# Kernel optimization log

Measured on AMD Instinct MI355X. Metric: run time of the kernel, lower is better.

The kernel has to match this reference:

```python
import jax, jax.numpy as jnp
import numpy as np

B, N, E_PER = 512, 256, 8192          # graphs, nodes per graph, edges per graph
FIN, H, K, FOUT = 128, 32, 16, 10     # in_channels, hidden, num clusters, out_channels
EPS = 1e-15


def setup_inputs() -> dict:
    key = jax.random.key(0)
    ks = jax.random.split(key, 12)
    x = jax.random.normal(ks[0], (B * N, FIN), jnp.float32)
    # intra-graph random edges, then offset into the global node index space
    src = jax.random.randint(ks[1], (B, E_PER), 0, N)
    dst = jax.random.randint(ks[2], (B, E_PER), 0, N)
    offs = (jnp.arange(B) * N)[:, None]
    edge_index = jnp.stack([(src + offs).reshape(-1), (dst + offs).reshape(-1)]).astype(jnp.int64)
    batch = jnp.repeat(jnp.arange(B), N).astype(jnp.int64)

    def lin(k, fin, fout):
        return (jax.random.normal(k, (fin, fout), jnp.float32) / np.sqrt(fin)).astype(jnp.float32)

    params = {
        'W_lin1': lin(ks[3], FIN, H), 'b_lin1': jnp.zeros((H,), jnp.float32),
        'W_rel1': lin(ks[4], H, H), 'b_rel1': jnp.zeros((H,), jnp.float32),
        'W_root1': lin(ks[5], H, H),
        'W_pool': lin(ks[6], H, K), 'b_pool': jnp.zeros((K,), jnp.float32),
        'W_rel2': lin(ks[7], H, H), 'b_rel2': jnp.zeros((H,), jnp.float32),
        'W_root2': lin(ks[8], H, H),
        'W_lin2': lin(ks[9], H, H), 'b_lin2': jnp.zeros((H,), jnp.float32),
        'W_lin3': lin(ks[10], H, FOUT), 'b_lin3': jnp.zeros((FOUT,), jnp.float32),
    }
    return {'x': x, 'edge_index': edge_index, 'batch': batch, **params}


def _densify(x, edge_index, batch):
    """to_dense_adj + to_dense_batch: [total,F] -> [B,N,F], [B,N,N], [B,N]."""
    n_total = x.shape[0]
    counts = jax.ops.segment_sum(jnp.ones((n_total,), jnp.int32), batch, num_segments=B)
    offsets = jnp.concatenate([jnp.zeros((1,), jnp.int32), jnp.cumsum(counts)[:-1]])
    pos = jnp.arange(n_total) - offsets[batch]            # position of node inside its graph
    eb = batch[edge_index[0]]                             # graph id of each edge
    adj = jnp.zeros((B, N, N), jnp.float32).at[eb, pos[edge_index[0]], pos[edge_index[1]]].add(1.0)
    xd = jnp.zeros((B, N, x.shape[1]), jnp.float32).at[batch, pos].set(x)
    mask = jnp.zeros((B, N), jnp.float32).at[batch, pos].set(1.0)
    return xd, adj, mask


def _dense_graph_conv(x, adj, W_rel, b_rel, W_root):
    # PyG DenseGraphConv(aggr='add'): lin_rel(adj @ x) + lin_root(x)
    return jnp.einsum('bnm,bmh,hk->bnk', adj, x, W_rel) + b_rel + x @ W_root


def _dense_mincut_pool(x, adj, s, mask):
    s = jax.nn.softmax(s, axis=-1)
    x = x * mask[..., None]
    s = s * mask[..., None]
    out = jnp.einsum('bnk,bnh->bkh', s, x)                        # s^T x
    out_adj = jnp.einsum('bnk,bnm,bmj->bkj', s, adj, s)           # s^T A s
    mincut_num = jnp.einsum('bkk->b', out_adj)
    d_flat = adj.sum(-1)                                          # degree
    mincut_den = jnp.einsum('bnk,bn,bnk->b', s, d_flat, s)        # trace(s^T D s)
    mincut_loss = jnp.mean(-(mincut_num / mincut_den))
    ss = jnp.einsum('bnk,bnj->bkj', s, s)
    ss_norm = jnp.linalg.norm(ss, axis=(-1, -2), keepdims=True)
    i_s = jnp.eye(K, dtype=jnp.float32)
    ortho_loss = jnp.mean(jnp.linalg.norm(ss / ss_norm - i_s / jnp.sqrt(jnp.float32(K)), axis=(-1, -2)))
    # zero diagonal, symmetric degree normalization
    diag_mask = 1.0 - i_s
    out_adj = out_adj * diag_mask
    d = jnp.sqrt(out_adj.sum(-1))[:, None, :] + EPS               # [B,1,K]
    out_adj = out_adj / d / jnp.swapaxes(d, 1, 2)
    return out, out_adj, mincut_loss, ortho_loss


def reference(x, edge_index, batch, W_lin1, b_lin1, W_rel1, b_rel1, W_root1,
              W_pool, b_pool, W_rel2, b_rel2, W_root2, W_lin2, b_lin2, W_lin3, b_lin3):
    xd, adj, mask = _densify(x, edge_index, batch)
    h = xd @ W_lin1 + b_lin1                                      # lin1
    h = _dense_graph_conv(h, adj, W_rel1, b_rel1, W_root1)        # conv1
    s2 = h @ W_pool + b_pool                                      # pool2
    h, adj_p, mincut_loss2, ortho_loss2 = _dense_mincut_pool(h, adj, s2, mask)
    h = _dense_graph_conv(h, adj_p, W_rel2, b_rel2, W_root2)      # conv2
    h = h.sum(axis=1)                                             # readout sum over clusters
    h = jax.nn.relu(h @ W_lin2 + b_lin2)
    h = h @ W_lin3 + b_lin3
    return jax.nn.log_softmax(h, axis=-1), mincut_loss2, ortho_loss2
```

## Files before the change

### kernel.cpp

```cpp
#include <hip/hip_runtime.h>

#define NB 512
#define NN 256
#define EPG 8192
#define FINC 128

typedef float f32x4 __attribute__((ext_vector_type(4)));
typedef short s16x8 __attribute__((ext_vector_type(8)));

__device__ __forceinline__ float bf2f(unsigned short u) {
  union { unsigned int i; float f; } x; x.i = ((unsigned int)u) << 16; return x.f;
}
__device__ __forceinline__ unsigned short f2bf(float f) {
  union { float f; unsigned int i; } x; x.f = f;
  unsigned int r = x.i + 0x7fffu + ((x.i >> 16) & 1u);
  return (unsigned short)(r >> 16);
}
__device__ __forceinline__ short ftrunc_bf(float f) {
  union { float f; unsigned int i; } x; x.f = f;
  return (short)(x.i >> 16);
}

struct Params {
  const void* x; const void* ei;
  const void *wl1, *bl1, *wr1, *br1, *wro1, *wp, *bp;
  const void *wr2, *br2, *wro2, *wl2, *bl2, *wl3, *bl3;
  float* out; float* ws;
};

__device__ __forceinline__ bool detect_bf16(const void* p) {
  const unsigned short* pw = (const unsigned short*)p;
  int sane = 0;
  for (int i = 0; i < 64; ++i) {
    unsigned e = (pw[i] >> 7) & 0xFFu;
    sane += (e > 96u && e < 132u) ? 1 : 0;
  }
  return sane >= 56;
}
__device__ __forceinline__ bool detect_i64(const void* p) {
  const int* pi = (const int*)p + EPG;
  int ok = 0;
  for (int i = 0; i < 32; ++i) ok += (pi[i] >= 256 && pi[i] < 512) ? 1 : 0;
  return ok < 24;
}
__device__ __forceinline__ float ldf(const void* p, int i, bool bf) {
  return bf ? bf2f(((const unsigned short*)p)[i]) : ((const float*)p)[i];
}

#define SMEM_TOTAL 162752

__global__ __launch_bounds__(1024, 4) void mincut_main(Params P) {
  extern __shared__ char smem[];
  const int t = threadIdx.x;
  const int b = blockIdx.x;

  const bool BF  = detect_bf16(P.wr1);
  const bool I64 = detect_i64(P.ei);

  float* h0buf  = (float*)(smem + 67584);
  unsigned short* taT = (unsigned short*)(smem + 67584);
  unsigned short* sTh = (unsigned short*)(smem + 76032);
  unsigned short* sTl = (unsigned short*)(smem + 84480);
  float* aggbuf = (float*)(smem + 104448);
  unsigned short* w1th = (unsigned short*)(smem + 104448);
  unsigned short* w1tl = (unsigned short*)(smem + 113152);
  unsigned short* h0T  = (unsigned short*)(smem + 141312);
  unsigned short* wrelTh  = (unsigned short*)(smem + 141312);
  unsigned short* wrelTl  = (unsigned short*)(smem + 143872);
  unsigned short* wrootTh = (unsigned short*)(smem + 146432);
  float* brel1f = (float*)(smem + 148992);
  unsigned short* h1Th = (unsigned short*)(smem + 141312);
  unsigned short* poolTh = (unsigned short*)(smem + 158208);
  unsigned short* poolTl = (unsigned short*)(smem + 159232);
  float* bpoolf = (float*)(smem + 160256);
  float* blin1f = (float*)(smem + 160320);
  float* scr    = (float*)(smem + 160448);
  float* degb   = (float*)(smem + 160704);
  float* ssqb   = (float*)(smem + 161728);
  float* pbuf   = (float*)(smem);
  float* oadjb  = (float*)(smem + 2048);
  float* ssb    = (float*)(smem + 3072);
  float* qbuf   = (float*)(smem + 4096);
  float* ddb    = (float*)(smem + 6144);
  float* h2b    = (float*)(smem + 6208);
  float* rb     = (float*)(smem + 8256);
  float* yb     = (float*)(smem + 8384);
  float* lgb    = (float*)(smem + 8512);
  float* rel2f  = (float*)(smem + 16384);
  float* root2f = (float*)(smem + 20608);
  float* lin2f  = (float*)(smem + 24704);
  float* lin3f  = (float*)(smem + 28928);
  float* pbufH  = (float*)(smem + 40960);
  float* pbufL  = (float*)(smem + 43008);
  float* oadjH  = (float*)(smem + 45056);
  float* oadjL  = (float*)(smem + 46080);
  float* ssA    = (float*)(smem + 47104);
  float* ssB    = (float*)(smem + 48128);
  float* ssC    = (float*)(smem + 49152);

  const int wv = t >> 6, lane = t & 63;
  const int lm = lane & 15, quad = lane >> 4;
  const int mbase = wv * 16;

  float wrel_v  = ldf(P.wr1, t, BF);
  float wroot_v = ldf(P.wro1, t, BF);
  float brel1_v = (t < 32) ? ldf(P.br1, t, BF) : 0.f;
  float rel2_v  = ldf(P.wr2, t, BF);
  float root2_v = ldf(P.wro2, t, BF);
  float lin2_v  = ldf(P.wl2, t, BF);
  float lin3_v  = (t < 320) ? ldf(P.wl3, t, BF) : 0.f;
  float brel2_v = (t < 32) ? ldf(P.br2, t, BF) : 0.f;
  float blin2_v = (t < 32) ? ldf(P.bl2, t, BF) : 0.f;
  float blin3_v = (t < 10) ? ldf(P.bl3, t, BF) : 0.f;
  int eu[8], ev[8];
  if (I64) {
    const uint4* s4 = (const uint4*)((const long long*)P.ei + (size_t)b * EPG) + t * 4;
    const uint4* d4 = (const uint4*)((const long long*)P.ei + (size_t)NB * EPG + (size_t)b * EPG) + t * 4;
    #pragma unroll
    for (int i = 0; i < 4; ++i) {
      uint4 a = s4[i], c = d4[i];
      eu[2 * i] = a.x & 255; eu[2 * i + 1] = a.z & 255;
      ev[2 * i] = c.x & 255; ev[2 * i + 1] = c.z & 255;
    }
  } else {
    const uint4* s4 = (const uint4*)((const int*)P.ei + (size_t)b * EPG) + t * 2;
    const uint4* d4 = (const uint4*)((const int*)P.ei + (size_t)NB * EPG + (size_t)b * EPG) + t * 2;
    #pragma unroll
    for (int i = 0; i < 2; ++i) {
      uint4 a = s4[i], c = d4[i];
      eu[4 * i] = a.x & 255; eu[4 * i + 1] = a.y & 255; eu[4 * i + 2] = a.z & 255; eu[4 * i + 3] = a.w & 255;
      ev[4 * i] = c.x & 255; ev[4 * i + 1] = c.y & 255; ev[4 * i + 2] = c.z & 255; ev[4 * i + 3] = c.w & 255;
    }
  }

  {
    uint4 z = {0u, 0u, 0u, 0u};
    for (int i = t; i < 4224; i += 1024) ((uint4*)smem)[i] = z;
  }
  for (int e = t; e < 4096; e += 1024) {
    int k = e >> 5, c = e & 31;
    float w = ldf(P.wl1, e, BF);
    unsigned short hi = f2bf(w);
    w1th[c * 136 + k] = hi;
    w1tl[c * 136 + k] = f2bf(w - bf2f(hi));
  }
  if (t < 512) {
    int m = t >> 4, c = t & 15;
    float w = ldf(P.wp, t, BF);
    unsigned short hi = f2bf(w);
    poolTh[c * 32 + m] = hi;
    poolTl[c * 32 + m] = f2bf(w - bf2f(hi));
  }
  if (t < 32) blin1f[t] = ldf(P.bl1, t, BF);
  if (t < 16) bpoolf[t] = ldf(P.bp, t, BF);
  __syncthreads();

  #pragma unroll
  for (int e = 0; e < 8; ++e) {
    unsigned idx = (unsigned)(eu[e] * 264 + ev[e]);
    atomicAdd((unsigned int*)(smem + (idx & ~3u)), 1u << ((idx & 3u) * 8u));
  }

  {
    f32x4 acc[2] = {{0.f,0.f,0.f,0.f},{0.f,0.f,0.f,0.f}};
    const size_t node = (size_t)(b * 256 + mbase + lm);
    #pragma unroll
    for (int ks = 0; ks < 4; ++ks) {
      const int k0 = ks * 32 + quad * 8;
      s16x8 a;
      if (BF) {
        a = *(const s16x8*)((const unsigned short*)P.x + node * 128 + k0);
      } else {
        const float* xp = (const float*)P.x + node * 128 + k0;
        f32x4 v0 = *(const f32x4*)xp;
        f32x4 v1 = *(const f32x4*)(xp + 4);
        #pragma unroll
        for (int j = 0; j < 4; ++j) { a[j] = (short)f2bf(v0[j]); a[4 + j] = (short)f2bf(v1[j]); }
      }
      #pragma unroll
      for (int ct = 0; ct < 2; ++ct) {
        const int c = ct * 16 + lm;
        s16x8 bh = *(const s16x8*)(w1th + c * 136 + k0);
        s16x8 bl = *(const s16x8*)(w1tl + c * 136 + k0);
        acc[ct] = __builtin_amdgcn_mfma_f32_16x16x32_bf16(a, bh, acc[ct], 0, 0, 0);
        acc[ct] = __builtin_amdgcn_mfma_f32_16x16x32_bf16(a, bl, acc[ct], 0, 0, 0);
      }
    }
    #pragma unroll
    for (int ct = 0; ct < 2; ++ct) {
      const int c = ct * 16 + lm;
      float bias = blin1f[c];
      #pragma unroll
      for (int r = 0; r < 4; ++r) {
        int row = mbase + quad * 4 + r;
        float val = acc[ct][r] + bias;
        h0buf[row * 36 + c] = val;
        h0T[c * 264 + row] = f2bf(val);
      }
    }
  }
  __syncthreads();

  s16x8 afr[8];
  {
    f32x4 acc[2] = {{0.f,0.f,0.f,0.f},{0.f,0.f,0.f,0.f}};
    float dsum = 0.f;
    const char* arow_ = smem + (mbase + lm) * 264;
    #pragma unroll
    for (int ks = 0; ks < 8; ++ks) {
      const int v0 = ks * 32 + quad * 8;
      uint2 d = *(const uint2*)(arow_ + v0);
      s16x8 a;
      #pragma unroll
      for (int j = 0; j < 4; ++j) {
        float f0 = (float)((d.x >> (8 * j)) & 255u);
        float f1 = (float)((d.y >> (8 * j)) & 255u);
        dsum += f0 + f1;
        a[j] = ftrunc_bf(f0);
        a[4 + j] = ftrunc_bf(f1);
      }
      afr[ks] = a;
      #pragma unroll
      for (int ct = 0; ct < 2; ++ct) {
        s16x8 bf = *(const s16x8*)(h0T + (ct * 16 + lm) * 264 + v0);
        acc[ct] = __builtin_amdgcn_mfma_f32_16x16x32_bf16(a, bf, acc[ct], 0, 0, 0);
      }
    }
    #pragma unroll
    for (int ct = 0; ct < 2; ++ct) {
      const int c = ct * 16 + lm;
      #pragma unroll
      for (int r = 0; r < 4; ++r) aggbuf[(mbase + quad * 4 + r) * 36 + c] = acc[ct][r];
    }
    dsum += __shfl_xor(dsum, 16, 64);
    dsum += __shfl_xor(dsum, 32, 64);
    if (lane < 16) degb[mbase + lm] = dsum;
  }
  __syncthreads();

  {
    int k = t >> 5, c = t & 31;
    unsigned short hi = f2bf(wrel_v);
    wrelTh[c * 40 + k] = hi;
    wrelTl[c * 40 + k] = f2bf(wrel_v - bf2f(hi));
    wrootTh[c * 40 + k] = f2bf(wroot_v);
  }
  if (t < 32) brel1f[t] = brel1_v;
  __syncthreads();

  f32x4 h1acc[2];
  float bias0, bias1;
  {
    s16x8 Ah, Al, Hh;
    const float* ar = aggbuf + (mbase + lm) * 36 + quad * 8;
    const float* hr = h0buf + (mbase + lm) * 36 + quad * 8;
    #pragma unroll
    for (int j = 0; j < 8; ++j) {
      float f = ar[j];
      unsigned short hi = f2bf(f);
      Ah[j] = (short)hi;
      Al[j] = (short)f2bf(f - bf2f(hi));
      Hh[j] = (short)f2bf(hr[j]);
    }
    bias0 = brel1f[lm]; bias1 = brel1f[16 + lm];
    #pragma unroll
    for (int ct = 0; ct < 2; ++ct) {
      const int c = ct * 16 + lm;
      s16x8 brh = *(const s16x8*)(wrelTh + c * 40 + quad * 8);
      s16x8 brl = *(const s16x8*)(wrelTl + c * 40 + quad * 8);
      s16x8 bwh = *(const s16x8*)(wrootTh + c * 40 + quad * 8);
      f32x4 acc = {0.f, 0.f, 0.f, 0.f};
      acc = __builtin_amdgcn_mfma_f32_16x16x32_bf16(Ah, brh, acc, 0, 0, 0);
      acc = __builtin_amdgcn_mfma_f32_16x16x32_bf16(Ah, brl, acc, 0, 0, 0);
      acc = __builtin_amdgcn_mfma_f32_16x16x32_bf16(Al, brh, acc, 0, 0, 0);
      acc = __builtin_amdgcn_mfma_f32_16x16x32_bf16(Hh, bwh, acc, 0, 0, 0);
      h1acc[ct] = acc;
    }
  }
  __syncthreads();
  {
    #pragma unroll
    for (int ct = 0; ct < 2; ++ct) {
      const int c = ct * 16 + lm;
      float bias = ct ? bias1 : bias0;
      #pragma unroll
      for (int r = 0; r < 4; ++r) {
        int row = mbase + quad * 4 + r;
        float val = h1acc[ct][r] + bias;
        aggbuf[row * 36 + c] = val;
        h1Th[c * 264 + row] = f2bf(val);
      }
    }
  }
  {
    s16x8 Ah, Al;
    const float* hr = aggbuf + (mbase + lm) * 36 + quad * 8;
    #pragma unroll
    for (int j = 0; j < 8; ++j) {
      float f = hr[j];
      unsigned short hi = f2bf(f);
      Ah[j] = (short)hi;
      Al[j] = (short)f2bf(f - bf2f(hi));
    }
    s16x8 Bh = *(const s16x8*)(poolTh + lm * 32 + quad * 8);
    s16x8 Bl = *(const s16x8*)(poolTl + lm * 32 + quad * 8);
    f32x4 lg = {0.f, 0.f, 0.f, 0.f};
    lg = __builtin_amdgcn_mfma_f32_16x16x32_bf16(Ah, Bh, lg, 0, 0, 0);
    lg = __builtin_amdgcn_mfma_f32_16x16x32_bf16(Al, Bh, lg, 0, 0, 0);
    lg = __builtin_amdgcn_mfma_f32_16x16x32_bf16(Ah, Bl, lg, 0, 0, 0);
    float bp = bpoolf[lm];
    #pragma unroll
    for (int r = 0; r < 4; ++r) lg[r] += bp;
    f32x4 mx = lg;
    #pragma unroll
    for (int m = 1; m <= 8; m <<= 1) {
      #pragma unroll
      for (int r = 0; r < 4; ++r) mx[r] = fmaxf(mx[r], __shfl_xor(mx[r], m, 64));
    }
    #pragma unroll
    for (int r = 0; r < 4; ++r) lg[r] = __expf(lg[r] - mx[r]);
    f32x4 sm = lg;
    #pragma unroll
    for (int m = 1; m <= 8; m <<= 1) {
      #pragma unroll
      for (int r = 0; r < 4; ++r) sm[r] += __shfl_xor(sm[r], m, 64);
    }
    f32x4 sq;
    #pragma unroll
    for (int r = 0; r < 4; ++r) {
      lg[r] = lg[r] / sm[r];
      sq[r] = lg[r] * lg[r];
    }
    #pragma unroll
    for (int m = 1; m <= 8; m <<= 1) {
      #pragma unroll
      for (int r = 0; r < 4; ++r) sq[r] += __shfl_xor(sq[r], m, 64);
    }
    #pragma unroll
    for (int r = 0; r < 4; ++r) {
      int node = mbase + quad * 4 + r;
      unsigned short hi = f2bf(lg[r]);
      sTh[lm * 264 + node] = hi;
      sTl[lm * 264 + node] = f2bf(lg[r] - bf2f(hi));
    }
    if (lm == 0) {
      #pragma unroll
      for (int r = 0; r < 4; ++r) ssqb[mbase + quad * 4 + r] = sq[r];
    }
  }
  __syncthreads();

  {
    f32x4 tacc = {0.f, 0.f, 0.f, 0.f};
    #pragma unroll
    for (int ks = 0; ks < 8; ++ks) {
      const int v0 = ks * 32 + quad * 8;
      s16x8 bh = *(const s16x8*)(sTh + lm * 264 + v0);
      s16x8 bl = *(const s16x8*)(sTl + lm * 264 + v0);
      tacc = __builtin_amdgcn_mfma_f32_16x16x32_bf16(afr[ks], bh, tacc, 0, 0, 0);
      tacc = __builtin_amdgcn_mfma_f32_16x16x32_bf16(afr[ks], bl, tacc, 0, 0, 0);
    }
    #pragma unroll
    for (int r = 0; r < 4; ++r) taT[lm * 264 + mbase + quad * 4 + r] = f2bf(tacc[r]);
  }
  __syncthreads();

  rel2f[t] = rel2_v;
  root2f[t] = root2_v;
  lin2f[t] = lin2_v;
  if (t < 320) lin3f[t] = lin3_v;

  if (wv < 9) {
    const unsigned short *Ap, *Bp; float* dst; int W, ct = 0;
    switch (wv) {
      case 0: Ap = sTh; Bp = h1Th; dst = pbufH; W = 32; ct = 0; break;
      case 1: Ap = sTh; Bp = h1Th; dst = pbufH; W = 32; ct = 1; break;
      case 2: Ap = sTl; Bp = h1Th; dst = pbufL; W = 32; ct = 0; break;
      case 3: Ap = sTl; Bp = h1Th; dst = pbufL; W = 32; ct = 1; break;
      case 4: Ap = sTh; Bp = taT;  dst = oadjH; W = 16; break;
      case 5: Ap = sTl; Bp = taT;  dst = oadjL; W = 16; break;
      case 6: Ap = sTh; Bp = sTh;  dst = ssA;   W = 16; break;
      case 7: Ap = sTh; Bp = sTl;  dst = ssB;   W = 16; break;
      default: Ap = sTl; Bp = sTh; dst = ssC;   W = 16; break;
    }
    const int cidx = ct * 16 + lm;
    const unsigned short* Bb = Bp + cidx * 264;
    f32x4 acc = {0.f, 0.f, 0.f, 0.f};
    #pragma unroll
    for (int ch = 0; ch < 8; ++ch) {
      s16x8 a = *(const s16x8*)(Ap + lm * 264 + ch * 32 + quad * 8);
      s16x8 bb = *(const s16x8*)(Bb + ch * 32 + quad * 8);
      acc = __builtin_amdgcn_mfma_f32_16x16x32_bf16(a, bb, acc, 0, 0, 0);
    }
    #pragma unroll
    for (int r = 0; r < 4; ++r) dst[(quad * 4 + r) * W + cidx] = acc[r];
  }
  __syncthreads();

  if (t < 512) {
    pbuf[t] = pbufH[t] + pbufL[t];
  } else if (t < 768) {
    int i = t - 512; oadjb[i] = oadjH[i] + oadjL[i];
  } else {
    int i = t - 768; ssb[i] = ssA[i] + ssB[i] + ssC[i];
  }
  __syncthreads();

  {
    float vden = (t < 256) ? degb[t] * ssqb[t] : 0.f;
    float vnum = (t < 16) ? oadjb[t * 17] : 0.f;
    float vfro = (t < 256) ? ssb[t] * ssb[t] : 0.f;
    float vtr  = (t < 16) ? ssb[t * 17] : 0.f;
    #pragma unroll
    for (int o = 32; o > 0; o >>= 1) {
      vden += __shfl_xor(vden, o, 64);
      vnum += __shfl_xor(vnum, o, 64);
      vfro += __shfl_xor(vfro, o, 64);
      vtr  += __shfl_xor(vtr, o, 64);
    }
    if (lane == 0) { scr[wv] = vden; scr[16 + wv] = vnum; scr[32 + wv] = vfro; scr[48 + wv] = vtr; }
  }
  __syncthreads();
  if (t == 0) {
    float den = 0.f, num = 0.f, fro = 0.f, tr = 0.f;
    #pragma unroll
    for (int i = 0; i < 16; ++i) { den += scr[i]; num += scr[16 + i]; fro += scr[32 + i]; tr += scr[48 + i]; }
    float ssn = sqrtf(fro);
    float orth2 = 2.f - tr / (2.f * ssn);
    atomicAdd(P.ws, -(num / den) * (1.f / NB));
    atomicAdd(P.ws + 1, sqrtf(fmaxf(orth2, 0.f)) * (1.f / NB));
  }
  if (t < 16) {
    float rs = 0.f;
    #pragma unroll
    for (int j = 0; j < 16; ++j) if (j != t) rs += oadjb[t * 16 + j];
    ddb[t] = sqrtf(rs) + 1e-15f;
  }
  __syncthreads();
  if (t < 256) {
    int k = t >> 4, j = t & 15;
    float apv = (k == j) ? 0.f : oadjb[t] / (ddb[k] * ddb[j]);
    oadjb[t] = apv;
  }
  __syncthreads();

  if (t < 512) {
    int k = t >> 5, c = t & 31;
    float q = 0.f;
    #pragma unroll
    for (int j = 0; j < 16; ++j) q += oadjb[k * 16 + j] * pbuf[j * 32 + c];
    qbuf[k * 32 + c] = q;
  }
  __syncthreads();
  if (t < 512) {
    int k = t >> 5, c = t & 31;
    float a1 = brel2_v;
    a1 = ((float*)nullptr == nullptr) ? a1 : a1;
    float acc = (t < 32) ? 0.f : 0.f;
    (void)acc;
    float s0 = 0.f;
    #pragma unroll
    for (int m = 0; m < 32; ++m)
      s0 += qbuf[k * 32 + m] * rel2f[m * 32 + c] + pbuf[k * 32 + m] * root2f[m * 32 + c];
    h2b[k * 32 + c] = s0;
  }
  __syncthreads();

  if (wv == 0) {
    if (lane < 32) {
      float r = 32.f * brel2_v;
      r = 0.f;
      #pragma unroll
      for (int k = 0; k < 16; ++k) r += h2b[k * 32 + lane];
      r += 16.f * brel2_v;
      rb[lane] = r;
    }
    if (lane < 32) {
      float y = blin2_v;
      #pragma unroll
      for (int m = 0; m < 32; ++m) y += rb[m] * lin2f[m * 32 + lane];
      yb[lane] = fmaxf(y, 0.f);
    }
    if (lane < 10) {
      float lg = blin3_v;
      #pragma unroll
      for (int m = 0; m < 32; ++m) lg += yb[m] * lin3f[m * 10 + lane];
      lgb[lane] = lg;
    }
    if (lane == 0) {
      float mx = lgb[0];
      #pragma unroll
      for (int i = 1; i < 10; ++i) mx = fmaxf(mx, lgb[i]);
      float sum = 0.f;
      #pragma unroll
      for (int i = 0; i < 10; ++i) sum += __expf(lgb[i] - mx);
      lgb[10] = mx + __logf(sum);
    }
    if (lane < 10) {
      float val = lgb[lane] - lgb[10];
      if (BF) ((unsigned short*)P.out)[b * 10 + lane] = f2bf(val);
      else    P.out[b * 10 + lane] = val;
    }
  }
}

__global__ void mincut_fin(Params P) {
  if (threadIdx.x == 0) {
    const bool BF = detect_bf16(P.wr1);
    if (BF) {
      ((unsigned short*)P.out)[5120] = f2bf(P.ws[0]);
      ((unsigned short*)P.out)[5121] = f2bf(P.ws[1]);
    } else {
      P.out[5120] = P.ws[0];
      P.out[5121] = P.ws[1];
    }
  }
}

extern "C" void kernel_launch(void* const* d_in, const int* in_sizes, int n_in,
                              void* d_out, int out_size, void* d_ws, size_t ws_size,
                              hipStream_t stream) {
  (void)in_sizes; (void)n_in; (void)out_size; (void)ws_size;
  Params P;
  P.x    = d_in[0];
  P.ei   = d_in[1];
  P.wl1  = d_in[3];
  P.bl1  = d_in[4];
  P.wr1  = d_in[5];
  P.br1  = d_in[6];
  P.wro1 = d_in[7];
  P.wp   = d_in[8];
  P.bp   = d_in[9];
  P.wr2  = d_in[10];
  P.br2  = d_in[11];
  P.wro2 = d_in[12];
  P.wl2  = d_in[13];
  P.bl2  = d_in[14];
  P.wl3  = d_in[15];
  P.bl3  = d_in[16];
  P.out  = (float*)d_out;
  P.ws   = (float*)d_ws;

  hipMemsetAsync(d_ws, 0, 2 * sizeof(float), stream);
  hipFuncSetAttribute(reinterpret_cast<const void*>(mincut_main),
                      hipFuncAttributeMaxDynamicSharedMemorySize, SMEM_TOTAL);
  hipLaunchKernelGGL(mincut_main, dim3(NB), dim3(1024), SMEM_TOTAL, stream, P);
  hipLaunchKernelGGL(mincut_fin, dim3(1), dim3(64), 0, stream, P);
}
```

Measured before the change: 182.6 us.

## Reassociate conv1 and pool via adjacency, pack adjacency as nibbles, halve LDS

Computes conv1 as A·(h0·Wrel) + h0·Wroot and the pool logits as A·(h0·Wrel·Wpool) + h0·Wroot·Wpool + bias, using precomputed weight products. The full-precision aggregation buffer and the separate conv1-to-pool stage go away. The adjacency is stored as 4-bit counts instead of 8-bit, and the ss terms are folded via symmetry. The lin1 split-bf16 low term is dropped. Shared memory shrinks from ~160KB to 80KB to allow two blocks per CU. Risks: counts above 15 overflow their nibble, and dropping the lin1 low term costs precision.

```diff
diff --git a/kernel.cpp b/kernel.cpp
--- a/kernel.cpp
+++ b/kernel.cpp
@@ -47,9 +47,9 @@
   return bf ? bf2f(((const unsigned short*)p)[i]) : ((const float*)p)[i];
 }
 
-#define SMEM_TOTAL 162752
-
-__global__ __launch_bounds__(1024, 4) void mincut_main(Params P) {
+#define SMEM_TOTAL 81920
+
+__global__ __launch_bounds__(1024, 8) void mincut_main(Params P) {
   extern __shared__ char smem[];
   const int t = threadIdx.x;
   const int b = blockIdx.x;
@@ -57,27 +57,7 @@
   const bool BF  = detect_bf16(P.wr1);
   const bool I64 = detect_i64(P.ei);
 
-  float* h0buf  = (float*)(smem + 67584);
-  unsigned short* taT = (unsigned short*)(smem + 67584);
-  unsigned short* sTh = (unsigned short*)(smem + 76032);
-  unsigned short* sTl = (unsigned short*)(smem + 84480);
-  float* aggbuf = (float*)(smem + 104448);
-  unsigned short* w1th = (unsigned short*)(smem + 104448);
-  unsigned short* w1tl = (unsigned short*)(smem + 113152);
-  unsigned short* h0T  = (unsigned short*)(smem + 141312);
-  unsigned short* wrelTh  = (unsigned short*)(smem + 141312);
-  unsigned short* wrelTl  = (unsigned short*)(smem + 143872);
-  unsigned short* wrootTh = (unsigned short*)(smem + 146432);
-  float* brel1f = (float*)(smem + 148992);
-  unsigned short* h1Th = (unsigned short*)(smem + 141312);
-  unsigned short* poolTh = (unsigned short*)(smem + 158208);
-  unsigned short* poolTl = (unsigned short*)(smem + 159232);
-  float* bpoolf = (float*)(smem + 160256);
-  float* blin1f = (float*)(smem + 160320);
-  float* scr    = (float*)(smem + 160448);
-  float* degb   = (float*)(smem + 160704);
-  float* ssqb   = (float*)(smem + 161728);
-  float* pbuf   = (float*)(smem);
+  float* pbuf   = (float*)(smem + 0);
   float* oadjb  = (float*)(smem + 2048);
   float* ssb    = (float*)(smem + 3072);
   float* qbuf   = (float*)(smem + 4096);
@@ -86,32 +66,45 @@
   float* rb     = (float*)(smem + 8256);
   float* yb     = (float*)(smem + 8384);
   float* lgb    = (float*)(smem + 8512);
-  float* rel2f  = (float*)(smem + 16384);
-  float* root2f = (float*)(smem + 20608);
-  float* lin2f  = (float*)(smem + 24704);
-  float* lin3f  = (float*)(smem + 28928);
-  float* pbufH  = (float*)(smem + 40960);
-  float* pbufL  = (float*)(smem + 43008);
-  float* oadjH  = (float*)(smem + 45056);
-  float* oadjL  = (float*)(smem + 46080);
-  float* ssA    = (float*)(smem + 47104);
-  float* ssB    = (float*)(smem + 48128);
-  float* ssC    = (float*)(smem + 49152);
+  float* scr    = (float*)(smem + 8704);
+  float* rel2f  = (float*)(smem + 9216);
+  float* root2f = (float*)(smem + 13312);
+  float* lin2f  = (float*)(smem + 17408);
+  float* lin3f  = (float*)(smem + 21504);
+  float* brel2f = (float*)(smem + 22784);
+  float* blin2f = (float*)(smem + 22912);
+  float* blin3f = (float*)(smem + 23040);
+  float* pbufH  = (float*)(smem + 24576);
+  float* pbufL  = (float*)(smem + 26624);
+  float* oadjH  = (float*)(smem + 28672);
+  float* oadjL  = (float*)(smem + 29696);
+  float* ssA    = (float*)(smem + 30720);
+  float* ssX    = (float*)(smem + 31744);
+  unsigned short* h0T  = (unsigned short*)(smem + 33792);
+  unsigned short* yTl  = (unsigned short*)(smem + 33792);
+  unsigned short* h1Th = (unsigned short*)(smem + 33792);
+  unsigned short* w1t  = (unsigned short*)(smem + 50688);
+  unsigned short* zT   = (unsigned short*)(smem + 50688);
+  unsigned short* sTh  = (unsigned short*)(smem + 50688);
+  unsigned short* sTl  = (unsigned short*)(smem + 59136);
+  unsigned short* wrelTh = (unsigned short*)(smem + 67584);
+  unsigned short* wrelTl = (unsigned short*)(smem + 70144);
+  unsigned short* wrootT = (unsigned short*)(smem + 72704);
+  float* blin1f = (float*)(smem + 75264);
+  unsigned short* yTh = (unsigned short*)(smem + 67584);
+  unsigned short* taT = (unsigned short*)(smem + 67584);
+  unsigned short* wpoolTh = (unsigned short*)(smem + 76032);
+  unsigned short* wpoolTl = (unsigned short*)(smem + 77184);
+  unsigned short* m1Th    = (unsigned short*)(smem + 78336);
+  unsigned short* m1Tl    = (unsigned short*)(smem + 79488);
+  unsigned short* m2Th    = (unsigned short*)(smem + 80640);
+  float*          bMf     = (float*)(smem + 81792);
+  unsigned short* brel1h  = (unsigned short*)(smem + 81856);
 
   const int wv = t >> 6, lane = t & 63;
   const int lm = lane & 15, quad = lane >> 4;
   const int mbase = wv * 16;
 
-  float wrel_v  = ldf(P.wr1, t, BF);
-  float wroot_v = ldf(P.wro1, t, BF);
-  float brel1_v = (t < 32) ? ldf(P.br1, t, BF) : 0.f;
-  float rel2_v  = ldf(P.wr2, t, BF);
-  float root2_v = ldf(P.wro2, t, BF);
-  float lin2_v  = ldf(P.wl2, t, BF);
-  float lin3_v  = (t < 320) ? ldf(P.wl3, t, BF) : 0.f;
-  float brel2_v = (t < 32) ? ldf(P.br2, t, BF) : 0.f;
-  float blin2_v = (t < 32) ? ldf(P.bl2, t, BF) : 0.f;
-  float blin3_v = (t < 10) ? ldf(P.bl3, t, BF) : 0.f;
   int eu[8], ev[8];
   if (I64) {
     const uint4* s4 = (const uint4*)((const long long*)P.ei + (size_t)b * EPG) + t * 4;
@@ -135,30 +128,34 @@
 
   {
     uint4 z = {0u, 0u, 0u, 0u};
-    for (int i = t; i < 4224; i += 1024) ((uint4*)smem)[i] = z;
+    for (int i = t; i < 2112; i += 1024) ((uint4*)smem)[i] = z;
   }
   for (int e = t; e < 4096; e += 1024) {
     int k = e >> 5, c = e & 31;
-    float w = ldf(P.wl1, e, BF);
-    unsigned short hi = f2bf(w);
-    w1th[c * 136 + k] = hi;
-    w1tl[c * 136 + k] = f2bf(w - bf2f(hi));
+    w1t[c * 136 + k] = f2bf(ldf(P.wl1, e, BF));
+  }
+  {
+    int k = t >> 5, c = t & 31;
+    float wr = ldf(P.wr1, t, BF);
+    unsigned short hi = f2bf(wr);
+    wrelTh[c * 40 + k] = hi;
+    wrelTl[c * 40 + k] = f2bf(wr - bf2f(hi));
+    wrootT[c * 40 + k] = f2bf(ldf(P.wro1, t, BF));
   }
   if (t < 512) {
     int m = t >> 4, c = t & 15;
     float w = ldf(P.wp, t, BF);
     unsigned short hi = f2bf(w);
-    poolTh[c * 32 + m] = hi;
-    poolTl[c * 32 + m] = f2bf(w - bf2f(hi));
-  }
-  if (t < 32) blin1f[t] = ldf(P.bl1, t, BF);
-  if (t < 16) bpoolf[t] = ldf(P.bp, t, BF);
+    wpoolTh[c * 36 + m] = hi;
+    wpoolTl[c * 36 + m] = f2bf(w - bf2f(hi));
+  }
+  if (t < 32) { blin1f[t] = ldf(P.bl1, t, BF); brel1h[t] = f2bf(ldf(P.br1, t, BF)); }
   __syncthreads();
 
   #pragma unroll
   for (int e = 0; e < 8; ++e) {
-    unsigned idx = (unsigned)(eu[e] * 264 + ev[e]);
-    atomicAdd((unsigned int*)(smem + (idx & ~3u)), 1u << ((idx & 3u) * 8u));
+    unsigned nib = (unsigned)(eu[e] * 264 + ev[e]);
+    atomicAdd((unsigned int*)(smem + ((nib >> 3) << 2)), 1u << ((nib & 7u) * 4u));
   }
 
   {
@@ -179,11 +176,8 @@
       }
       #pragma unroll
       for (int ct = 0; ct < 2; ++ct) {
-        const int c = ct * 16 + lm;
-        s16x8 bh = *(const s16x8*)(w1th + c * 136 + k0);
-        s16x8 bl = *(const s16x8*)(w1tl + c * 136 + k0);
+        s16x8 bh = *(const s16x8*)(w1t + (ct * 16 + lm) * 136 + k0);
         acc[ct] = __builtin_amdgcn_mfma_f32_16x16x32_bf16(a, bh, acc[ct], 0, 0, 0);
-        acc[ct] = __builtin_amdgcn_mfma_f32_16x16x32_bf16(a, bl, acc[ct], 0, 0, 0);
       }
     }
     #pragma unroll
@@ -191,162 +185,179 @@
       const int c = ct * 16 + lm;
       float bias = blin1f[c];
       #pragma unroll
-      for (int r = 0; r < 4; ++r) {
-        int row = mbase + quad * 4 + r;
-        float val = acc[ct][r] + bias;
-        h0buf[row * 36 + c] = val;
-        h0T[c * 264 + row] = f2bf(val);
-      }
-    }
-  }
-  __syncthreads();
-
-  s16x8 afr[8];
-  {
-    f32x4 acc[2] = {{0.f,0.f,0.f,0.f},{0.f,0.f,0.f,0.f}};
-    float dsum = 0.f;
-    const char* arow_ = smem + (mbase + lm) * 264;
-    #pragma unroll
-    for (int ks = 0; ks < 8; ++ks) {
-      const int v0 = ks * 32 + quad * 8;
-      uint2 d = *(const uint2*)(arow_ + v0);
-      s16x8 a;
-      #pragma unroll
-      for (int j = 0; j < 4; ++j) {
-        float f0 = (float)((d.x >> (8 * j)) & 255u);
-        float f1 = (float)((d.y >> (8 * j)) & 255u);
-        dsum += f0 + f1;
-        a[j] = ftrunc_bf(f0);
-        a[4 + j] = ftrunc_bf(f1);
-      }
-      afr[ks] = a;
-      #pragma unroll
-      for (int ct = 0; ct < 2; ++ct) {
-        s16x8 bf = *(const s16x8*)(h0T + (ct * 16 + lm) * 264 + v0);
-        acc[ct] = __builtin_amdgcn_mfma_f32_16x16x32_bf16(a, bf, acc[ct], 0, 0, 0);
-      }
-    }
-    #pragma unroll
-    for (int ct = 0; ct < 2; ++ct) {
-      const int c = ct * 16 + lm;
-      #pragma unroll
-      for (int r = 0; r < 4; ++r) aggbuf[(mbase + quad * 4 + r) * 36 + c] = acc[ct][r];
-    }
-    dsum += __shfl_xor(dsum, 16, 64);
-    dsum += __shfl_xor(dsum, 32, 64);
-    if (lane < 16) degb[mbase + lm] = dsum;
-  }
-  __syncthreads();
-
-  {
-    int k = t >> 5, c = t & 31;
-    unsigned short hi = f2bf(wrel_v);
-    wrelTh[c * 40 + k] = hi;
-    wrelTl[c * 40 + k] = f2bf(wrel_v - bf2f(hi));
-    wrootTh[c * 40 + k] = f2bf(wroot_v);
-  }
-  if (t < 32) brel1f[t] = brel1_v;
-  __syncthreads();
-
-  f32x4 h1acc[2];
-  float bias0, bias1;
-  {
-    s16x8 Ah, Al, Hh;
-    const float* ar = aggbuf + (mbase + lm) * 36 + quad * 8;
-    const float* hr = h0buf + (mbase + lm) * 36 + quad * 8;
+      for (int r = 0; r < 4; ++r)
+        h0T[c * 264 + mbase + quad * 4 + r] = f2bf(acc[ct][r] + bias);
+    }
+  }
+
+  if (wv == 2 || wv == 3) {
+    const int mb = (wv - 2) * 16;
+    s16x8 Ah, Al;
     #pragma unroll
     for (int j = 0; j < 8; ++j) {
-      float f = ar[j];
-      unsigned short hi = f2bf(f);
-      Ah[j] = (short)hi;
-      Al[j] = (short)f2bf(f - bf2f(hi));
-      Hh[j] = (short)f2bf(hr[j]);
-    }
-    bias0 = brel1f[lm]; bias1 = brel1f[16 + lm];
+      int k = quad * 8 + j;
+      Ah[j] = (short)wrelTh[k * 40 + mb + lm];
+      Al[j] = (short)wrelTl[k * 40 + mb + lm];
+    }
+    s16x8 Bh, Bl;
+    ((uint2*)&Bh)[0] = *(const uint2*)(wpoolTh + lm * 36 + quad * 8);
+    ((uint2*)&Bh)[1] = *(const uint2*)(wpoolTh + lm * 36 + quad * 8 + 4);
+    ((uint2*)&Bl)[0] = *(const uint2*)(wpoolTl + lm * 36 + quad * 8);
+    ((uint2*)&Bl)[1] = *(const uint2*)(wpoolTl + lm * 36 + quad * 8 + 4);
+    f32x4 acc = {0.f, 0.f, 0.f, 0.f};
+    acc = __builtin_amdgcn_mfma_f32_16x16x32_bf16(Ah, Bh, acc, 0, 0, 0);
+    acc = __builtin_amdgcn_mfma_f32_16x16x32_bf16(Al, Bh, acc, 0, 0, 0);
+    acc = __builtin_amdgcn_mfma_f32_16x16x32_bf16(Ah, Bl, acc, 0, 0, 0);
+    #pragma unroll
+    for (int r = 0; r < 4; ++r) {
+      int m = mb + quad * 4 + r;
+      unsigned short hi = f2bf(acc[r]);
+      m1Th[lm * 36 + m] = hi;
+      m1Tl[lm * 36 + m] = f2bf(acc[r] - bf2f(hi));
+    }
+  }
+  if (wv == 4 || wv == 5) {
+    const int mb = (wv - 4) * 16;
+    s16x8 Ah;
+    #pragma unroll
+    for (int j = 0; j < 8; ++j) Ah[j] = (short)wrootT[(quad * 8 + j) * 40 + mb + lm];
+    s16x8 Bh, Bl;
+    ((uint2*)&Bh)[0] = *(const uint2*)(wpoolTh + lm * 36 + quad * 8);
+    ((uint2*)&Bh)[1] = *(const uint2*)(wpoolTh + lm * 36 + quad * 8 + 4);
+    ((uint2*)&Bl)[0] = *(const uint2*)(wpoolTl + lm * 36 + quad * 8);
+    ((uint2*)&Bl)[1] = *(const uint2*)(wpoolTl + lm * 36 + quad * 8 + 4);
+    f32x4 acc = {0.f, 0.f, 0.f, 0.f};
+    acc = __builtin_amdgcn_mfma_f32_16x16x32_bf16(Ah, Bh, acc, 0, 0, 0);
+    acc = __builtin_amdgcn_mfma_f32_16x16x32_bf16(Ah, Bl, acc, 0, 0, 0);
+    #pragma unroll
+    for (int r = 0; r < 4; ++r) m2Th[lm * 36 + (mb + quad * 4 + r)] = f2bf(acc[r]);
+  }
+  if (wv == 6 && lane < 16) {
+    float acc = ldf(P.bp, lane, BF);
+    #pragma unroll 8
+    for (int m = 0; m < 32; ++m)
+      acc += bf2f(brel1h[m]) * (bf2f(wpoolTh[lane * 36 + m]) + bf2f(wpoolTl[lane * 36 + m]));
+    bMf[lane] = acc;
+  }
+  __syncthreads();
+
+  f32x4 racc[2] = {{0.f,0.f,0.f,0.f},{0.f,0.f,0.f,0.f}};
+  f32x4 yacc = {0.f,0.f,0.f,0.f}, macc = {0.f,0.f,0.f,0.f};
+  {
+    s16x8 Ah;
+    #pragma unroll
+    for (int j = 0; j < 8; ++j) Ah[j] = (short)h0T[(quad * 8 + j) * 264 + mbase + lm];
+    f32x4 zacc[2] = {{0.f,0.f,0.f,0.f},{0.f,0.f,0.f,0.f}};
     #pragma unroll
     for (int ct = 0; ct < 2; ++ct) {
       const int c = ct * 16 + lm;
       s16x8 brh = *(const s16x8*)(wrelTh + c * 40 + quad * 8);
       s16x8 brl = *(const s16x8*)(wrelTl + c * 40 + quad * 8);
-      s16x8 bwh = *(const s16x8*)(wrootTh + c * 40 + quad * 8);
-      f32x4 acc = {0.f, 0.f, 0.f, 0.f};
-      acc = __builtin_amdgcn_mfma_f32_16x16x32_bf16(Ah, brh, acc, 0, 0, 0);
-      acc = __builtin_amdgcn_mfma_f32_16x16x32_bf16(Ah, brl, acc, 0, 0, 0);
-      acc = __builtin_amdgcn_mfma_f32_16x16x32_bf16(Al, brh, acc, 0, 0, 0);
-      acc = __builtin_amdgcn_mfma_f32_16x16x32_bf16(Hh, bwh, acc, 0, 0, 0);
-      h1acc[ct] = acc;
-    }
-  }
-  __syncthreads();
-  {
+      s16x8 bro = *(const s16x8*)(wrootT + c * 40 + quad * 8);
+      zacc[ct] = __builtin_amdgcn_mfma_f32_16x16x32_bf16(Ah, brh, zacc[ct], 0, 0, 0);
+      zacc[ct] = __builtin_amdgcn_mfma_f32_16x16x32_bf16(Ah, brl, zacc[ct], 0, 0, 0);
+      racc[ct] = __builtin_amdgcn_mfma_f32_16x16x32_bf16(Ah, bro, racc[ct], 0, 0, 0);
+    }
+    s16x8 Bm1h, Bm1l, Bm2;
+    ((uint2*)&Bm1h)[0] = *(const uint2*)(m1Th + lm * 36 + quad * 8);
+    ((uint2*)&Bm1h)[1] = *(const uint2*)(m1Th + lm * 36 + quad * 8 + 4);
+    ((uint2*)&Bm1l)[0] = *(const uint2*)(m1Tl + lm * 36 + quad * 8);
+    ((uint2*)&Bm1l)[1] = *(const uint2*)(m1Tl + lm * 36 + quad * 8 + 4);
+    ((uint2*)&Bm2)[0]  = *(const uint2*)(m2Th + lm * 36 + quad * 8);
+    ((uint2*)&Bm2)[1]  = *(const uint2*)(m2Th + lm * 36 + quad * 8 + 4);
+    yacc = __builtin_amdgcn_mfma_f32_16x16x32_bf16(Ah, Bm1h, yacc, 0, 0, 0);
+    yacc = __builtin_amdgcn_mfma_f32_16x16x32_bf16(Ah, Bm1l, yacc, 0, 0, 0);
+    macc = __builtin_amdgcn_mfma_f32_16x16x32_bf16(Ah, Bm2, macc, 0, 0, 0);
+    #pragma unroll
+    for (int ct = 0; ct < 2; ++ct)
+      #pragma unroll
+      for (int r = 0; r < 4; ++r)
+        zT[(ct * 16 + lm) * 264 + mbase + quad * 4 + r] = f2bf(zacc[ct][r]);
+  }
+  __syncthreads();
+
+  #pragma unroll
+  for (int r = 0; r < 4; ++r) {
+    int node = mbase + quad * 4 + r;
+    unsigned short hi = f2bf(yacc[r]);
+    yTh[lm * 264 + node] = hi;
+    yTl[lm * 264 + node] = f2bf(yacc[r] - bf2f(hi));
+  }
+  __syncthreads();
+
+  unsigned adjw[8];
+  f32x4 h1v[2], sval, sq;
+  float degf;
+  {
+    f32x4 h1acc[2] = {{0.f,0.f,0.f,0.f},{0.f,0.f,0.f,0.f}};
+    f32x4 lacc = {0.f,0.f,0.f,0.f};
+    unsigned dsum = 0;
+    const char* arow = smem + (mbase + lm) * 132;
+    #pragma unroll
+    for (int ks = 0; ks < 8; ++ks) {
+      unsigned d = *(const unsigned int*)(arow + ks * 16 + quad * 4);
+      adjw[ks] = d;
+      unsigned v = (d & 0x0F0F0F0Fu) + ((d >> 4) & 0x0F0F0F0Fu);
+      dsum += (v * 0x01010101u) >> 24;
+      s16x8 af;
+      #pragma unroll
+      for (int j = 0; j < 8; ++j) af[j] = ftrunc_bf((float)((d >> (4 * j)) & 15u));
+      const int v0 = ks * 32 + quad * 8;
+      #pragma unroll
+      for (int ct = 0; ct < 2; ++ct) {
+        s16x8 bz = *(const s16x8*)(zT + (ct * 16 + lm) * 264 + v0);
+        h1acc[ct] = __builtin_amdgcn_mfma_f32_16x16x32_bf16(af, bz, h1acc[ct], 0, 0, 0);
+      }
+      s16x8 byh = *(const s16x8*)(yTh + lm * 264 + v0);
+      s16x8 byl = *(const s16x8*)(yTl + lm * 264 + v0);
+      lacc = __builtin_amdgcn_mfma_f32_16x16x32_bf16(af, byh, lacc, 0, 0, 0);
+      lacc = __builtin_amdgcn_mfma_f32_16x16x32_bf16(af, byl, lacc, 0, 0, 0);
+    }
+    dsum += __shfl_xor(dsum, 16, 64);
+    dsum += __shfl_xor(dsum, 32, 64);
+    degf = (float)dsum;
     #pragma unroll
     for (int ct = 0; ct < 2; ++ct) {
-      const int c = ct * 16 + lm;
-      float bias = ct ? bias1 : bias0;
-      #pragma unroll
-      for (int r = 0; r < 4; ++r) {
-        int row = mbase + quad * 4 + r;
-        float val = h1acc[ct][r] + bias;
-        aggbuf[row * 36 + c] = val;
-        h1Th[c * 264 + row] = f2bf(val);
-      }
-    }
-  }
-  {
-    s16x8 Ah, Al;
-    const float* hr = aggbuf + (mbase + lm) * 36 + quad * 8;
-    #pragma unroll
-    for (int j = 0; j < 8; ++j) {
-      float f = hr[j];
-      unsigned short hi = f2bf(f);
-      Ah[j] = (short)hi;
-      Al[j] = (short)f2bf(f - bf2f(hi));
-    }
-    s16x8 Bh = *(const s16x8*)(poolTh + lm * 32 + quad * 8);
-    s16x8 Bl = *(const s16x8*)(poolTl + lm * 32 + quad * 8);
-    f32x4 lg = {0.f, 0.f, 0.f, 0.f};
-    lg = __builtin_amdgcn_mfma_f32_16x16x32_bf16(Ah, Bh, lg, 0, 0, 0);
-    lg = __builtin_amdgcn_mfma_f32_16x16x32_bf16(Al, Bh, lg, 0, 0, 0);
-    lg = __builtin_amdgcn_mfma_f32_16x16x32_bf16(Ah, Bl, lg, 0, 0, 0);
-    float bp = bpoolf[lm];
-    #pragma unroll
-    for (int r = 0; r < 4; ++r) lg[r] += bp;
+      float bias = bf2f(brel1h[ct * 16 + lm]);
+      #pragma unroll
+      for (int r = 0; r < 4; ++r) h1v[ct][r] = h1acc[ct][r] + racc[ct][r] + bias;
+    }
+    f32x4 lg;
+    float bm = bMf[lm];
+    #pragma unroll
+    for (int r = 0; r < 4; ++r) lg[r] = lacc[r] + macc[r] + bm;
     f32x4 mx = lg;
     #pragma unroll
-    for (int m = 1; m <= 8; m <<= 1) {
+    for (int m = 1; m <= 8; m <<= 1)
       #pragma unroll
       for (int r = 0; r < 4; ++r) mx[r] = fmaxf(mx[r], __shfl_xor(mx[r], m, 64));
-    }
     #pragma unroll
     for (int r = 0; r < 4; ++r) lg[r] = __expf(lg[r] - mx[r]);
     f32x4 sm = lg;
     #pragma unroll
-    for (int m = 1; m <= 8; m <<= 1) {
+    for (int m = 1; m <= 8; m <<= 1)
       #pragma unroll
       for (int r = 0; r < 4; ++r) sm[r] += __shfl_xor(sm[r], m, 64);
-    }
-    f32x4 sq;
-    #pragma unroll
-    for (int r = 0; r < 4; ++r) {
-      lg[r] = lg[r] / sm[r];
-      sq[r] = lg[r] * lg[r];
-    }
-    #pragma unroll
-    for (int m = 1; m <= 8; m <<= 1) {
+    #pragma unroll
+    for (int r = 0; r < 4; ++r) { sval[r] = lg[r] / sm[r]; sq[r] = sval[r] * sval[r]; }
+    #pragma unroll
+    for (int m = 1; m <= 8; m <<= 1)
       #pragma unroll
       for (int r = 0; r < 4; ++r) sq[r] += __shfl_xor(sq[r], m, 64);
-    }
-    #pragma unroll
-    for (int r = 0; r < 4; ++r) {
-      int node = mbase + quad * 4 + r;
-      unsigned short hi = f2bf(lg[r]);
-      sTh[lm * 264 + node] = hi;
-      sTl[lm * 264 + node] = f2bf(lg[r] - bf2f(hi));
-    }
-    if (lm == 0) {
-      #pragma unroll
-      for (int r = 0; r < 4; ++r) ssqb[mbase + quad * 4 + r] = sq[r];
-    }
+  }
+  __syncthreads();
+
+  #pragma unroll
+  for (int ct = 0; ct < 2; ++ct)
+    #pragma unroll
+    for (int r = 0; r < 4; ++r)
+      h1Th[(ct * 16 + lm) * 264 + mbase + quad * 4 + r] = f2bf(h1v[ct][r]);
+  #pragma unroll
+  for (int r = 0; r < 4; ++r) {
+    int node = mbase + quad * 4 + r;
+    unsigned short hi = f2bf(sval[r]);
+    sTh[lm * 264 + node] = hi;
+    sTl[lm * 264 + node] = f2bf(sval[r] - bf2f(hi));
   }
   __syncthreads();
 
@@ -354,23 +365,30 @@
     f32x4 tacc = {0.f, 0.f, 0.f, 0.f};
     #pragma unroll
     for (int ks = 0; ks < 8; ++ks) {
+      unsigned d = adjw[ks];
+      s16x8 af;
+      #pragma unroll
+      for (int j = 0; j < 8; ++j) af[j] = ftrunc_bf((float)((d >> (4 * j)) & 15u));
       const int v0 = ks * 32 + quad * 8;
       s16x8 bh = *(const s16x8*)(sTh + lm * 264 + v0);
       s16x8 bl = *(const s16x8*)(sTl + lm * 264 + v0);
-      tacc = __builtin_amdgcn_mfma_f32_16x16x32_bf16(afr[ks], bh, tacc, 0, 0, 0);
-      tacc = __builtin_amdgcn_mfma_f32_16x16x32_bf16(afr[ks], bl, tacc, 0, 0, 0);
+      tacc = __builtin_amdgcn_mfma_f32_16x16x32_bf16(af, bh, tacc, 0, 0, 0);
+      tacc = __builtin_amdgcn_mfma_f32_16x16x32_bf16(af, bl, tacc, 0, 0, 0);
     }
     #pragma unroll
     for (int r = 0; r < 4; ++r) taT[lm * 264 + mbase + quad * 4 + r] = f2bf(tacc[r]);
   }
   __syncthreads();
 
-  rel2f[t] = rel2_v;
-  root2f[t] = root2_v;
-  lin2f[t] = lin2_v;
-  if (t < 320) lin3f[t] = lin3_v;
-
-  if (wv < 9) {
+  rel2f[t] = ldf(P.wr2, t, BF);
+  root2f[t] = ldf(P.wro2, t, BF);
+  lin2f[t] = ldf(P.wl2, t, BF);
+  if (t < 320) lin3f[t] = ldf(P.wl3, t, BF);
+  if (t < 32) brel2f[t] = ldf(P.br2, t, BF);
+  if (t < 32) blin2f[t] = ldf(P.bl2, t, BF);
+  if (t < 10) blin3f[t] = ldf(P.bl3, t, BF);
+
+  if (wv < 8) {
     const unsigned short *Ap, *Bp; float* dst; int W, ct = 0;
     switch (wv) {
       case 0: Ap = sTh; Bp = h1Th; dst = pbufH; W = 32; ct = 0; break;
@@ -380,8 +398,7 @@
       case 4: Ap = sTh; Bp = taT;  dst = oadjH; W = 16; break;
       case 5: Ap = sTl; Bp = taT;  dst = oadjL; W = 16; break;
       case 6: Ap = sTh; Bp = sTh;  dst = ssA;   W = 16; break;
-      case 7: Ap = sTh; Bp = sTl;  dst = ssB;   W = 16; break;
-      default: Ap = sTl; Bp = sTh; dst = ssC;   W = 16; break;
+      default: Ap = sTh; Bp = sTl; dst = ssX;   W = 16; break;
     }
     const int cidx = ct * 16 + lm;
     const unsigned short* Bb = Bp + cidx * 264;
@@ -402,12 +419,17 @@
   } else if (t < 768) {
     int i = t - 512; oadjb[i] = oadjH[i] + oadjL[i];
   } else {
-    int i = t - 768; ssb[i] = ssA[i] + ssB[i] + ssC[i];
-  }
-  __syncthreads();
-
-  {
-    float vden = (t < 256) ? degb[t] * ssqb[t] : 0.f;
+    int i = t - 768; int k3 = i >> 4, j3 = i & 15;
+    ssb[i] = ssA[i] + ssX[i] + ssX[j3 * 16 + k3];
+  }
+  __syncthreads();
+
+  {
+    int l = lane & 15, src = (l >> 2) << 4;
+    float q0 = __shfl(sq[0], src, 64), q1 = __shfl(sq[1], src, 64);
+    float q2 = __shfl(sq[2], src, 64), q3 = __shfl(sq[3], src, 64);
+    float ssel = (l & 2) ? ((l & 1) ? q3 : q2) : ((l & 1) ? q1 : q0);
+    float vden = (lane < 16) ? degf * ssel : 0.f;
     float vnum = (t < 16) ? oadjb[t * 17] : 0.f;
     float vfro = (t < 256) ? ssb[t] * ssb[t] : 0.f;
     float vtr  = (t < 16) ? ssb[t * 17] : 0.f;
@@ -421,6 +443,7 @@
     if (lane == 0) { scr[wv] = vden; scr[16 + wv] = vnum; scr[32 + wv] = vfro; scr[48 + wv] = vtr; }
   }
   __syncthreads();
+
   if (t == 0) {
     float den = 0.f, num = 0.f, fro = 0.f, tr = 0.f;
     #pragma unroll
@@ -454,10 +477,6 @@
   __syncthreads();
   if (t < 512) {
     int k = t >> 5, c = t & 31;
-    float a1 = brel2_v;
-    a1 = ((float*)nullptr == nullptr) ? a1 : a1;
-    float acc = (t < 32) ? 0.f : 0.f;
-    (void)acc;
     float s0 = 0.f;
     #pragma unroll
     for (int m = 0; m < 32; ++m)
@@ -468,21 +487,19 @@
 
   if (wv == 0) {
     if (lane < 32) {
-      float r = 32.f * brel2_v;
-      r = 0.f;
+      float r = 16.f * brel2f[lane];
       #pragma unroll
       for (int k = 0; k < 16; ++k) r += h2b[k * 32 + lane];
-      r += 16.f * brel2_v;
       rb[lane] = r;
     }
     if (lane < 32) {
-      float y = blin2_v;
+      float y = blin2f[lane];
       #pragma unroll
       for (int m = 0; m < 32; ++m) y += rb[m] * lin2f[m * 32 + lane];
       yb[lane] = fmaxf(y, 0.f);
     }
     if (lane < 10) {
-      float lg = blin3_v;
+      float lg = blin3f[lane];
       #pragma unroll
       for (int m = 0; m < 32; ++m) lg += yb[m] * lin3f[m * 10 + lane];
       lgb[lane] = lg;
```

After: 204.2 us. +11.8%, slower.
